# Kernel tuning notes

Measured on AMD Instinct MI355X. Metric: run time of the kernel, lower is better.

## Reference

```python
import jax, jax.numpy as jnp
import numpy as np

B, S, D, H = 2, 2048, 1024, 16
HD = D // H  # 64
MASK_VAL = -10000.0


def setup_inputs() -> dict:
    key = jax.random.key(0)
    ks = jax.random.split(key, 8)
    sc = 0.02
    q_features = jax.random.normal(ks[0], (B, S, D), jnp.float32)
    kv_features = jax.random.normal(ks[1], (B, S, D), jnp.float32)
    # causal mask, broadcastable (1,1,S,S)
    mask = jnp.tril(jnp.ones((S, S), jnp.bool_))[None, None]
    Wq = jax.random.normal(ks[2], (D, D), jnp.float32) * sc
    bq = jnp.zeros((D,), jnp.float32)
    Wkv = jax.random.normal(ks[3], (D, 2 * D), jnp.float32) * sc
    bkv = jnp.zeros((2 * D,), jnp.float32)
    Wp = jax.random.normal(ks[4], (D, D), jnp.float32) * sc
    bp = jnp.zeros((D,), jnp.float32)
    return {"q_features": q_features, "kv_features": kv_features, "mask": mask,
            "Wq": Wq, "bq": bq, "Wkv": Wkv, "bkv": bkv, "Wp": Wp, "bp": bp}


def _split_heads(t):
    # (B,S,D) -> (B,H,S,HD)
    return t.reshape(B, S, H, HD).transpose(0, 2, 1, 3)


def reference(q_features, kv_features, mask, Wq, bq, Wkv, bkv, Wp, bp):
    query = q_features @ Wq + bq            # (B,S,D)
    kv = kv_features @ Wkv + bkv            # (B,S,2D)
    key, value = jnp.split(kv, 2, axis=-1)
    q = _split_heads(query)                 # (B,H,S,HD)
    k = _split_heads(key)
    v = _split_heads(value)
    scores = jnp.einsum('bhqd,bhkd->bhqk', q, k) / jnp.sqrt(jnp.float32(HD))
    scores = jnp.where(mask, scores, jnp.asarray(MASK_VAL, scores.dtype))
    attn = jax.nn.softmax(scores, axis=-1)  # (B,H,S,S)
    out = jnp.einsum('bhqk,bhkd->bhqd', attn, v)
    out = out.transpose(0, 2, 1, 3).reshape(B, S, D)  # merge heads
    return out @ Wp + bp
```

## Files before the change

### kernel.cpp

```cpp
#include <hip/hip_runtime.h>

typedef unsigned short u16;
typedef unsigned int u32;
typedef __attribute__((ext_vector_type(4))) unsigned short us4;
typedef __attribute__((ext_vector_type(8))) unsigned short us8;
typedef __attribute__((ext_vector_type(8))) __bf16 bf16x8;
typedef __attribute__((ext_vector_type(4))) float floatx4;

#define S_ 2048
#define D_ 1024

__device__ __forceinline__ u16 f2bf(float f) {
  unsigned u = __builtin_bit_cast(unsigned, f);
  unsigned r = (u + 0x7fffu + ((u >> 16) & 1u)) >> 16;
  return (u16)r;
}

typedef const __attribute__((address_space(1))) u32* gas_t;
typedef __attribute__((address_space(3))) u32* las_t;
__device__ __forceinline__ void gload16(const u16* g, u16* l) {
  __builtin_amdgcn_global_load_lds((gas_t)g, (las_t)l, 16, 0, 0);
}

__global__ __launch_bounds__(256) void prep(
    const float* __restrict__ qf, const float* __restrict__ kvf,
    const float* __restrict__ Wq, const float* __restrict__ Wkv,
    const float* __restrict__ Wp, u16* __restrict__ qa, u16* __restrict__ kva,
    u16* __restrict__ Wqt, u16* __restrict__ Wkvt, u16* __restrict__ Wpt) {
  int bid = blockIdx.x, tid = threadIdx.x;
  if (bid < 4096) {
    const float* src = (bid < 2048) ? qf : kvf;
    u16* dst = (bid < 2048) ? qa : kva;
    size_t i = ((size_t)(bid & 2047) * 256 + tid) * 8;
    floatx4 a = *(const floatx4*)(src + i);
    floatx4 b = *(const floatx4*)(src + i + 4);
    us8 r;
#pragma unroll
    for (int j = 0; j < 4; j++) { r[j] = f2bf(a[j]); r[4 + j] = f2bf(b[j]); }
    *(us8*)(dst + i) = r;
  } else {
    int t = bid - 4096;
    const float* src; u16* dst; int R, C;
    if (t < 1024)      { src = Wq;  dst = Wqt;  R = 1024; C = 1024; }
    else if (t < 3072) { t -= 1024; src = Wkv; dst = Wkvt; R = 1024; C = 2048; }
    else               { t -= 3072; src = Wp;  dst = Wpt;  R = 1024; C = 1024; }
    int bx = t % (C >> 5), by = t / (C >> 5);
    __shared__ u16 tile[32][33];
    int tx = tid & 31, ty = tid >> 5;
    int x = bx * 32 + tx;
    for (int i = ty; i < 32; i += 8)
      tile[i][tx] = f2bf(src[(size_t)(by * 32 + i) * C + x]);
    __syncthreads();
    int ox = by * 32 + tx;
    for (int i = ty; i < 32; i += 8)
      dst[(size_t)(bx * 32 + i) * R + ox] = tile[tx][i];
  }
}

__device__ __forceinline__ void gemm_core(
    const u16* __restrict__ A, const u16* __restrict__ Bt,
    const float* __restrict__ bias, void* __restrict__ C0,
    u16* __restrict__ C1, int N, int mode, int n0, int m0,
    u16* As, u16* Bs) {
  int tid  = threadIdx.x;
  int wave = tid >> 6, lane = tid & 63;
  int quad = lane >> 4, l16 = lane & 15;
  int wr = wave >> 1, wc = wave & 1;
  const u16* Ag = A  + (size_t)(m0 + wave * 8 + (lane >> 3)) * 1024 + (lane & 7) * 8;
  const u16* Bg = Bt + (size_t)(n0 + wave * 8 + (lane >> 3)) * 1024 + (lane & 7) * 8;
  u16* Aw = As + wave * 8 * 64;
  u16* Bw = Bs + wave * 8 * 64;
  floatx4 acc[4][4] = {};
  for (int k0 = 0; k0 < 1024; k0 += 64) {
    if (k0) __syncthreads();
#pragma unroll
    for (int p = 0; p < 4; p++) {
      gload16(Ag + (size_t)p * 32 * 1024 + k0, Aw + p * 32 * 64);
      gload16(Bg + (size_t)p * 32 * 1024 + k0, Bw + p * 32 * 64);
    }
    __syncthreads();
#pragma unroll
    for (int kk = 0; kk < 2; kk++) {
      bf16x8 af[4], bf[4];
#pragma unroll
      for (int mt = 0; mt < 4; mt++)
        af[mt] = __builtin_bit_cast(bf16x8,
            *(const us8*)&As[(wr * 64 + mt * 16 + l16) * 64 + (kk * 4 + quad) * 8]);
#pragma unroll
      for (int nt = 0; nt < 4; nt++)
        bf[nt] = __builtin_bit_cast(bf16x8,
            *(const us8*)&Bs[(wc * 64 + nt * 16 + l16) * 64 + (kk * 4 + quad) * 8]);
#pragma unroll
      for (int mt = 0; mt < 4; mt++)
#pragma unroll
        for (int nt = 0; nt < 4; nt++)
          acc[mt][nt] = __builtin_amdgcn_mfma_f32_16x16x32_bf16(
              af[mt], bf[nt], acc[mt][nt], 0, 0, 0);
    }
  }
#pragma unroll
  for (int mt = 0; mt < 4; mt++) {
#pragma unroll
    for (int nt = 0; nt < 4; nt++) {
      int col  = n0 + wc * 64 + nt * 16 + l16;
      int rowq = m0 + wr * 64 + mt * 16 + quad * 4;
      float bv = bias[col];
      if (mode == 0) {
        u16* o = (u16*)C0;
#pragma unroll
        for (int r = 0; r < 4; r++)
          o[(size_t)(rowq + r) * N + col] = f2bf(acc[mt][nt][r] + bv);
      } else if (mode == 1) {
        float* o = (float*)C0;
#pragma unroll
        for (int r = 0; r < 4; r++)
          o[(size_t)(rowq + r) * N + col] = acc[mt][nt][r] + bv;
      } else {
        if (col < 1024) {
          u16* o = (u16*)C0;
#pragma unroll
          for (int r = 0; r < 4; r++)
            o[(size_t)(rowq + r) * 1024 + col] = f2bf(acc[mt][nt][r] + bv);
        } else {
          int vcol = col - 1024;
          int b = rowq >> 11, s0 = rowq & 2047;
          us4 pv;
#pragma unroll
          for (int r = 0; r < 4; r++) pv[r] = f2bf(acc[mt][nt][r] + bv);
          *(us4*)&C1[((size_t)(b * 1024 + vcol)) * (size_t)S_ + s0] = pv;
        }
      }
    }
  }
}

__global__ __launch_bounds__(256) void gemm_qkv(
    const u16* __restrict__ qa, const u16* __restrict__ kva,
    const u16* __restrict__ Wqt, const u16* __restrict__ Wkvt,
    const float* __restrict__ bq, const float* __restrict__ bkv,
    u16* __restrict__ Qb, u16* __restrict__ Kb, u16* __restrict__ Vt) {
  __shared__ __align__(16) u16 As[128 * 64];
  __shared__ __align__(16) u16 Bs[128 * 64];
  int bid = blockIdx.x;
  if (bid < 256) {
    gemm_core(qa, Wqt, bq, Qb, nullptr, 1024, 0,
              (bid & 7) * 128, (bid >> 3) * 128, As, Bs);
  } else {
    int lb = bid - 256;
    gemm_core(kva, Wkvt, bkv, Kb, Vt, 2048, 2,
              (lb & 15) * 128, (lb >> 4) * 128, As, Bs);
  }
}

__global__ __launch_bounds__(256) void gemm_out(
    const u16* __restrict__ AO, const u16* __restrict__ Wpt,
    const float* __restrict__ bp, float* __restrict__ out) {
  __shared__ __align__(16) u16 As[128 * 64];
  __shared__ __align__(16) u16 Bs[128 * 64];
  gemm_core(AO, Wpt, bp, out, nullptr, 1024, 1,
            (blockIdx.x & 7) * 128, (blockIdx.x >> 3) * 128, As, Bs);
}

__global__ __launch_bounds__(256) void attn_fwd(
    const u16* __restrict__ Q, const u16* __restrict__ Kb,
    const u16* __restrict__ Vt, u16* __restrict__ O) {
  __shared__ __align__(16) u16 Ks[2][64 * 64];
  __shared__ __align__(16) u16 Vs[2][64 * 64];
  __shared__ __align__(16) u16 Ps[4][16 * 72];
  int tid  = threadIdx.x;
  int wave = tid >> 6, lane = tid & 63;
  int quad = lane >> 4, l16 = lane & 15;
  int bh = blockIdx.x, b = bh >> 4, h = bh & 15;
  const size_t row0 = (size_t)b * S_;
  const u16* Kg = Kb + row0 * D_ + h * 64;
  const u16* Vg = Vt + ((size_t)b * 1024 + h * 64) * S_;
  int sr8 = tid >> 3, sc8 = tid & 7;

  for (int seg = 0; seg < 2; seg++) {
    int qt = seg ? (31 - blockIdx.y) : blockIdx.y;
    int qrow = qt * 64 + wave * 16 + l16;
    const u16* qp = Q + (row0 + qrow) * D_ + h * 64 + quad * 8;
    bf16x8 aqv[2];
    aqv[0] = __builtin_bit_cast(bf16x8, *(const us8*)(qp));
    aqv[1] = __builtin_bit_cast(bf16x8, *(const us8*)(qp + 32));

    float m_[4] = {-1e9f, -1e9f, -1e9f, -1e9f};
    float l_[4] = {0.f, 0.f, 0.f, 0.f};
    floatx4 o_[4] = {};

    __syncthreads();
#pragma unroll
    for (int rr = 0; rr < 2; rr++) {
      int r8 = sr8 + rr * 32;
      us8 k8 = *(const us8*)(Kg + (size_t)r8 * D_ + sc8 * 8);
      *(us8*)&Ks[0][r8 * 64 + ((sc8 ^ (r8 & 7)) << 3)] = k8;
      us8 v8 = *(const us8*)(Vg + (size_t)r8 * S_ + sc8 * 8);
      *(us8*)&Vs[0][r8 * 64 + ((sc8 ^ (r8 & 7)) << 3)] = v8;
    }

    for (int kb = 0; kb <= qt; kb++) {
      __syncthreads();
      int cur = kb & 1;
      bool pre = kb < qt;
      us8 pk0, pk1, pv0, pv1;
      if (pre) {
        int koff = (kb + 1) * 64;
        pk0 = *(const us8*)(Kg + (size_t)(koff + sr8) * D_ + sc8 * 8);
        pk1 = *(const us8*)(Kg + (size_t)(koff + sr8 + 32) * D_ + sc8 * 8);
        pv0 = *(const us8*)(Vg + (size_t)sr8 * S_ + koff + sc8 * 8);
        pv1 = *(const us8*)(Vg + (size_t)(sr8 + 32) * S_ + koff + sc8 * 8);
      }

      floatx4 s[4] = {};
#pragma unroll
      for (int kk = 0; kk < 2; kk++)
#pragma unroll
        for (int nt = 0; nt < 4; nt++) {
          int key = nt * 16 + l16;
          us8 kf = *(const us8*)&Ks[cur][key * 64 + (((kk * 4 + quad) ^ (l16 & 7)) << 3)];
          s[nt] = __builtin_amdgcn_mfma_f32_16x16x32_bf16(
              aqv[kk], __builtin_bit_cast(bf16x8, kf), s[nt], 0, 0, 0);
        }

      bool diag = (kb == qt);
#pragma unroll
      for (int nt = 0; nt < 4; nt++)
#pragma unroll
        for (int r = 0; r < 4; r++) {
          float v = s[nt][r] * 0.125f;
          if (diag) {
            int qg = wave * 16 + quad * 4 + r;
            int kg = nt * 16 + l16;
            if (kg > qg) v = -10000.0f;
          }
          s[nt][r] = v;
        }

      float mnew[4], alpha[4];
#pragma unroll
      for (int r = 0; r < 4; r++) {
        float rm = fmaxf(fmaxf(s[0][r], s[1][r]), fmaxf(s[2][r], s[3][r]));
        rm = fmaxf(rm, __shfl_xor(rm, 1));
        rm = fmaxf(rm, __shfl_xor(rm, 2));
        rm = fmaxf(rm, __shfl_xor(rm, 4));
        rm = fmaxf(rm, __shfl_xor(rm, 8));
        mnew[r] = fmaxf(m_[r], rm);
        alpha[r] = __expf(m_[r] - mnew[r]);
        m_[r] = mnew[r];
      }

#pragma unroll
      for (int nt = 0; nt < 4; nt++)
#pragma unroll
        for (int r = 0; r < 4; r++) {
          float p = __expf(s[nt][r] - mnew[r]);
          s[nt][r] = p;
          Ps[wave][(quad * 4 + r) * 72 + nt * 16 + l16] = f2bf(p);
        }
#pragma unroll
      for (int r = 0; r < 4; r++) {
        float rs = s[0][r] + s[1][r] + s[2][r] + s[3][r];
        rs += __shfl_xor(rs, 1);
        rs += __shfl_xor(rs, 2);
        rs += __shfl_xor(rs, 4);
        rs += __shfl_xor(rs, 8);
        l_[r] = l_[r] * alpha[r] + rs;
        o_[0][r] *= alpha[r];
        o_[1][r] *= alpha[r];
        o_[2][r] *= alpha[r];
        o_[3][r] *= alpha[r];
      }

#pragma unroll
      for (int kk = 0; kk < 2; kk++) {
        us8 pa = *(const us8*)&Ps[wave][l16 * 72 + (kk * 4 + quad) * 8];
        bf16x8 pav = __builtin_bit_cast(bf16x8, pa);
#pragma unroll
        for (int nt = 0; nt < 4; nt++) {
          int hd = nt * 16 + l16;
          us8 vf = *(const us8*)&Vs[cur][hd * 64 + (((kk * 4 + quad) ^ (l16 & 7)) << 3)];
          o_[nt] = __builtin_amdgcn_mfma_f32_16x16x32_bf16(
              pav, __builtin_bit_cast(bf16x8, vf), o_[nt], 0, 0, 0);
        }
      }

      if (pre) {
        int nxt = cur ^ 1;
        *(us8*)&Ks[nxt][sr8 * 64 + ((sc8 ^ (sr8 & 7)) << 3)] = pk0;
        *(us8*)&Ks[nxt][(sr8 + 32) * 64 + ((sc8 ^ (sr8 & 7)) << 3)] = pk1;
        *(us8*)&Vs[nxt][sr8 * 64 + ((sc8 ^ (sr8 & 7)) << 3)] = pv0;
        *(us8*)&Vs[nxt][(sr8 + 32) * 64 + ((sc8 ^ (sr8 & 7)) << 3)] = pv1;
      }
    }

#pragma unroll
    for (int nt = 0; nt < 4; nt++) {
      int col = h * 64 + nt * 16 + l16;
#pragma unroll
      for (int r = 0; r < 4; r++) {
        size_t row = row0 + qt * 64 + wave * 16 + quad * 4 + r;
        O[row * D_ + col] = f2bf(o_[nt][r] / l_[r]);
      }
    }
  }
}

extern "C" void kernel_launch(void* const* d_in, const int* in_sizes, int n_in,
                              void* d_out, int out_size, void* d_ws, size_t ws_size,
                              hipStream_t stream) {
  const float* qf  = (const float*)d_in[0];
  const float* kvf = (const float*)d_in[1];
  const float* Wq  = (const float*)d_in[3];
  const float* bq  = (const float*)d_in[4];
  const float* Wkv = (const float*)d_in[5];
  const float* bkv = (const float*)d_in[6];
  const float* Wp  = (const float*)d_in[7];
  const float* bp  = (const float*)d_in[8];

  char* ws = (char*)d_ws;
  const size_t MB = 1048576;
  u16* kva  = (u16*)(ws);
  u16* AO   = (u16*)(ws);
  u16* Kbp  = (u16*)(ws + 8 * MB);
  u16* Vtp  = (u16*)(ws + 16 * MB);
  u16* Wqt  = (u16*)(ws + 24 * MB);
  u16* Wkvt = (u16*)(ws + 26 * MB);
  u16* Wpt  = (u16*)(ws + 30 * MB);
  u16* qa   = (u16*)d_out;
  u16* Qb   = (u16*)d_out + (size_t)4 * 1048576;

  prep<<<8192, 256, 0, stream>>>(qf, kvf, Wq, Wkv, Wp, qa, kva, Wqt, Wkvt, Wpt);
  gemm_qkv<<<768, 256, 0, stream>>>(qa, kva, Wqt, Wkvt, bq, bkv, Qb, Kbp, Vtp);
  attn_fwd<<<dim3(32, 16), 256, 0, stream>>>(Qb, Kbp, Vtp, AO);
  gemm_out<<<256, 256, 0, stream>>>(AO, Wpt, bp, (float*)d_out);
}
```

Baseline: 252.7 us.

## Fold softmax scale into Q projection, use exp2, retile attention and output GEMM

The Q projection epilogue now multiplies by log2(e)/sqrt(64), so attention drops the per-score multiply and uses the hardware exp2 instruction. Attention runs one query tile per block with a grid of 32x32 instead of two balanced segments per block, and it uses single-buffered K/V with an extra barrier. The output GEMM is templated to 64x128 tiles and launches 512 blocks for better CU occupancy. Other small changes are round-half-up bf16 conversion for P and a reciprocal instead of a divide. Dropping the causal load-balancing pairing may leave the workload across blocks uneven, and the tail rounds can idle CUs.

After: 267.1 us. +5.7%, slower.

```diff
diff --git a/kernel.cpp b/kernel.cpp
--- a/kernel.cpp
+++ b/kernel.cpp
@@ -9,11 +9,15 @@
 
 #define S_ 2048
 #define D_ 1024
+#define QSC 0.18033688f
 
 __device__ __forceinline__ u16 f2bf(float f) {
   unsigned u = __builtin_bit_cast(unsigned, f);
   unsigned r = (u + 0x7fffu + ((u >> 16) & 1u)) >> 16;
   return (u16)r;
+}
+__device__ __forceinline__ u16 f2bf_rhu(float f) {
+  return (u16)((__builtin_bit_cast(unsigned, f) + 0x8000u) >> 16);
 }
 
 typedef const __attribute__((address_space(1))) u32* gas_t;
@@ -57,11 +61,13 @@
   }
 }
 
+template <int TM, int TN, int MODE>
 __device__ __forceinline__ void gemm_core(
     const u16* __restrict__ A, const u16* __restrict__ Bt,
     const float* __restrict__ bias, void* __restrict__ C0,
-    u16* __restrict__ C1, int N, int mode, int n0, int m0,
-    u16* As, u16* Bs) {
+    u16* __restrict__ C1, int N, int n0, int m0,
+    u16* As, u16* Bs, float cscale) {
+  constexpr int MT = TM / 32, NT = TN / 32;
   int tid  = threadIdx.x;
   int wave = tid >> 6, lane = tid & 63;
   int quad = lane >> 4, l16 = lane & 15;
@@ -70,47 +76,48 @@
   const u16* Bg = Bt + (size_t)(n0 + wave * 8 + (lane >> 3)) * 1024 + (lane & 7) * 8;
   u16* Aw = As + wave * 8 * 64;
   u16* Bw = Bs + wave * 8 * 64;
-  floatx4 acc[4][4] = {};
+  floatx4 acc[MT][NT] = {};
   for (int k0 = 0; k0 < 1024; k0 += 64) {
     if (k0) __syncthreads();
 #pragma unroll
-    for (int p = 0; p < 4; p++) {
+    for (int p = 0; p < TM / 32; p++)
       gload16(Ag + (size_t)p * 32 * 1024 + k0, Aw + p * 32 * 64);
+#pragma unroll
+    for (int p = 0; p < TN / 32; p++)
       gload16(Bg + (size_t)p * 32 * 1024 + k0, Bw + p * 32 * 64);
-    }
     __syncthreads();
 #pragma unroll
     for (int kk = 0; kk < 2; kk++) {
-      bf16x8 af[4], bf[4];
-#pragma unroll
-      for (int mt = 0; mt < 4; mt++)
+      bf16x8 af[MT], bf[NT];
+#pragma unroll
+      for (int mt = 0; mt < MT; mt++)
         af[mt] = __builtin_bit_cast(bf16x8,
-            *(const us8*)&As[(wr * 64 + mt * 16 + l16) * 64 + (kk * 4 + quad) * 8]);
-#pragma unroll
-      for (int nt = 0; nt < 4; nt++)
+            *(const us8*)&As[(wr * (TM / 2) + mt * 16 + l16) * 64 + (kk * 4 + quad) * 8]);
+#pragma unroll
+      for (int nt = 0; nt < NT; nt++)
         bf[nt] = __builtin_bit_cast(bf16x8,
-            *(const us8*)&Bs[(wc * 64 + nt * 16 + l16) * 64 + (kk * 4 + quad) * 8]);
-#pragma unroll
-      for (int mt = 0; mt < 4; mt++)
-#pragma unroll
-        for (int nt = 0; nt < 4; nt++)
+            *(const us8*)&Bs[(wc * (TN / 2) + nt * 16 + l16) * 64 + (kk * 4 + quad) * 8]);
+#pragma unroll
+      for (int mt = 0; mt < MT; mt++)
+#pragma unroll
+        for (int nt = 0; nt < NT; nt++)
           acc[mt][nt] = __builtin_amdgcn_mfma_f32_16x16x32_bf16(
               af[mt], bf[nt], acc[mt][nt], 0, 0, 0);
     }
   }
 #pragma unroll
-  for (int mt = 0; mt < 4; mt++) {
-#pragma unroll
-    for (int nt = 0; nt < 4; nt++) {
-      int col  = n0 + wc * 64 + nt * 16 + l16;
-      int rowq = m0 + wr * 64 + mt * 16 + quad * 4;
+  for (int mt = 0; mt < MT; mt++) {
+#pragma unroll
+    for (int nt = 0; nt < NT; nt++) {
+      int col  = n0 + wc * (TN / 2) + nt * 16 + l16;
+      int rowq = m0 + wr * (TM / 2) + mt * 16 + quad * 4;
       float bv = bias[col];
-      if (mode == 0) {
+      if (MODE == 0) {
         u16* o = (u16*)C0;
 #pragma unroll
         for (int r = 0; r < 4; r++)
-          o[(size_t)(rowq + r) * N + col] = f2bf(acc[mt][nt][r] + bv);
-      } else if (mode == 1) {
+          o[(size_t)(rowq + r) * N + col] = f2bf((acc[mt][nt][r] + bv) * cscale);
+      } else if (MODE == 1) {
         float* o = (float*)C0;
 #pragma unroll
         for (int r = 0; r < 4; r++)
@@ -143,164 +150,160 @@
   __shared__ __align__(16) u16 Bs[128 * 64];
   int bid = blockIdx.x;
   if (bid < 256) {
-    gemm_core(qa, Wqt, bq, Qb, nullptr, 1024, 0,
-              (bid & 7) * 128, (bid >> 3) * 128, As, Bs);
+    gemm_core<128, 128, 0>(qa, Wqt, bq, Qb, nullptr, 1024,
+                           (bid & 7) * 128, (bid >> 3) * 128, As, Bs, QSC);
   } else {
     int lb = bid - 256;
-    gemm_core(kva, Wkvt, bkv, Kb, Vt, 2048, 2,
-              (lb & 15) * 128, (lb >> 4) * 128, As, Bs);
+    gemm_core<128, 128, 2>(kva, Wkvt, bkv, Kb, Vt, 2048,
+                           (lb & 15) * 128, (lb >> 4) * 128, As, Bs, 1.0f);
   }
 }
 
 __global__ __launch_bounds__(256) void gemm_out(
     const u16* __restrict__ AO, const u16* __restrict__ Wpt,
     const float* __restrict__ bp, float* __restrict__ out) {
-  __shared__ __align__(16) u16 As[128 * 64];
+  __shared__ __align__(16) u16 As[64 * 64];
   __shared__ __align__(16) u16 Bs[128 * 64];
-  gemm_core(AO, Wpt, bp, out, nullptr, 1024, 1,
-            (blockIdx.x & 7) * 128, (blockIdx.x >> 3) * 128, As, Bs);
+  gemm_core<64, 128, 1>(AO, Wpt, bp, out, nullptr, 1024,
+                        (blockIdx.x & 7) * 128, (blockIdx.x >> 3) * 64, As, Bs, 1.0f);
 }
 
 __global__ __launch_bounds__(256) void attn_fwd(
     const u16* __restrict__ Q, const u16* __restrict__ Kb,
     const u16* __restrict__ Vt, u16* __restrict__ O) {
-  __shared__ __align__(16) u16 Ks[2][64 * 64];
-  __shared__ __align__(16) u16 Vs[2][64 * 64];
+  __shared__ __align__(16) u16 Ks[64 * 64];
+  __shared__ __align__(16) u16 Vs[64 * 64];
   __shared__ __align__(16) u16 Ps[4][16 * 72];
   int tid  = threadIdx.x;
   int wave = tid >> 6, lane = tid & 63;
   int quad = lane >> 4, l16 = lane & 15;
   int bh = blockIdx.x, b = bh >> 4, h = bh & 15;
+  int qt = blockIdx.y;
   const size_t row0 = (size_t)b * S_;
   const u16* Kg = Kb + row0 * D_ + h * 64;
   const u16* Vg = Vt + ((size_t)b * 1024 + h * 64) * S_;
   int sr8 = tid >> 3, sc8 = tid & 7;
 
-  for (int seg = 0; seg < 2; seg++) {
-    int qt = seg ? (31 - blockIdx.y) : blockIdx.y;
-    int qrow = qt * 64 + wave * 16 + l16;
-    const u16* qp = Q + (row0 + qrow) * D_ + h * 64 + quad * 8;
-    bf16x8 aqv[2];
-    aqv[0] = __builtin_bit_cast(bf16x8, *(const us8*)(qp));
-    aqv[1] = __builtin_bit_cast(bf16x8, *(const us8*)(qp + 32));
-
-    float m_[4] = {-1e9f, -1e9f, -1e9f, -1e9f};
-    float l_[4] = {0.f, 0.f, 0.f, 0.f};
-    floatx4 o_[4] = {};
-
+  int qrow = qt * 64 + wave * 16 + l16;
+  const u16* qp = Q + (row0 + qrow) * D_ + h * 64 + quad * 8;
+  bf16x8 aqv[2];
+  aqv[0] = __builtin_bit_cast(bf16x8, *(const us8*)(qp));
+  aqv[1] = __builtin_bit_cast(bf16x8, *(const us8*)(qp + 32));
+
+  float m_[4] = {-1e9f, -1e9f, -1e9f, -1e9f};
+  float l_[4] = {0.f, 0.f, 0.f, 0.f};
+  floatx4 o_[4] = {};
+
+#pragma unroll
+  for (int rr = 0; rr < 2; rr++) {
+    int r8 = sr8 + rr * 32;
+    us8 k8 = *(const us8*)(Kg + (size_t)r8 * D_ + sc8 * 8);
+    *(us8*)&Ks[r8 * 64 + ((sc8 ^ (r8 & 7)) << 3)] = k8;
+    us8 v8 = *(const us8*)(Vg + (size_t)r8 * S_ + sc8 * 8);
+    *(us8*)&Vs[r8 * 64 + ((sc8 ^ (r8 & 7)) << 3)] = v8;
+  }
+
+  for (int kb = 0; kb <= qt; kb++) {
     __syncthreads();
-#pragma unroll
-    for (int rr = 0; rr < 2; rr++) {
-      int r8 = sr8 + rr * 32;
-      us8 k8 = *(const us8*)(Kg + (size_t)r8 * D_ + sc8 * 8);
-      *(us8*)&Ks[0][r8 * 64 + ((sc8 ^ (r8 & 7)) << 3)] = k8;
-      us8 v8 = *(const us8*)(Vg + (size_t)r8 * S_ + sc8 * 8);
-      *(us8*)&Vs[0][r8 * 64 + ((sc8 ^ (r8 & 7)) << 3)] = v8;
-    }
-
-    for (int kb = 0; kb <= qt; kb++) {
-      __syncthreads();
-      int cur = kb & 1;
-      bool pre = kb < qt;
-      us8 pk0, pk1, pv0, pv1;
-      if (pre) {
-        int koff = (kb + 1) * 64;
-        pk0 = *(const us8*)(Kg + (size_t)(koff + sr8) * D_ + sc8 * 8);
-        pk1 = *(const us8*)(Kg + (size_t)(koff + sr8 + 32) * D_ + sc8 * 8);
-        pv0 = *(const us8*)(Vg + (size_t)sr8 * S_ + koff + sc8 * 8);
-        pv1 = *(const us8*)(Vg + (size_t)(sr8 + 32) * S_ + koff + sc8 * 8);
+    bool pre = kb < qt;
+    us8 pk0, pk1, pv0, pv1;
+    if (pre) {
+      int koff = (kb + 1) * 64;
+      pk0 = *(const us8*)(Kg + (size_t)(koff + sr8) * D_ + sc8 * 8);
+      pk1 = *(const us8*)(Kg + (size_t)(koff + sr8 + 32) * D_ + sc8 * 8);
+      pv0 = *(const us8*)(Vg + (size_t)sr8 * S_ + koff + sc8 * 8);
+      pv1 = *(const us8*)(Vg + (size_t)(sr8 + 32) * S_ + koff + sc8 * 8);
+    }
+
+    floatx4 s[4] = {};
+#pragma unroll
+    for (int kk = 0; kk < 2; kk++)
+#pragma unroll
+      for (int nt = 0; nt < 4; nt++) {
+        int key = nt * 16 + l16;
+        us8 kf = *(const us8*)&Ks[key * 64 + (((kk * 4 + quad) ^ (l16 & 7)) << 3)];
+        s[nt] = __builtin_amdgcn_mfma_f32_16x16x32_bf16(
+            aqv[kk], __builtin_bit_cast(bf16x8, kf), s[nt], 0, 0, 0);
       }
 
-      floatx4 s[4] = {};
-#pragma unroll
-      for (int kk = 0; kk < 2; kk++)
-#pragma unroll
-        for (int nt = 0; nt < 4; nt++) {
-          int key = nt * 16 + l16;
-          us8 kf = *(const us8*)&Ks[cur][key * 64 + (((kk * 4 + quad) ^ (l16 & 7)) << 3)];
-          s[nt] = __builtin_amdgcn_mfma_f32_16x16x32_bf16(
-              aqv[kk], __builtin_bit_cast(bf16x8, kf), s[nt], 0, 0, 0);
+    if (kb == qt) {
+#pragma unroll
+      for (int nt = 0; nt < 4; nt++)
+#pragma unroll
+        for (int r = 0; r < 4; r++) {
+          int qg = wave * 16 + quad * 4 + r;
+          int kg = nt * 16 + l16;
+          if (kg > qg) s[nt][r] = -1e5f;
         }
-
-      bool diag = (kb == qt);
-#pragma unroll
-      for (int nt = 0; nt < 4; nt++)
-#pragma unroll
-        for (int r = 0; r < 4; r++) {
-          float v = s[nt][r] * 0.125f;
-          if (diag) {
-            int qg = wave * 16 + quad * 4 + r;
-            int kg = nt * 16 + l16;
-            if (kg > qg) v = -10000.0f;
-          }
-          s[nt][r] = v;
-        }
-
-      float mnew[4], alpha[4];
+    }
+
+    float mnew[4], alpha[4];
+#pragma unroll
+    for (int r = 0; r < 4; r++) {
+      float rm = fmaxf(fmaxf(s[0][r], s[1][r]), fmaxf(s[2][r], s[3][r]));
+      rm = fmaxf(rm, __shfl_xor(rm, 1));
+      rm = fmaxf(rm, __shfl_xor(rm, 2));
+      rm = fmaxf(rm, __shfl_xor(rm, 4));
+      rm = fmaxf(rm, __shfl_xor(rm, 8));
+      mnew[r] = fmaxf(m_[r], rm);
+      alpha[r] = __builtin_amdgcn_exp2f(m_[r] - mnew[r]);
+      m_[r] = mnew[r];
+    }
+
+#pragma unroll
+    for (int nt = 0; nt < 4; nt++)
 #pragma unroll
       for (int r = 0; r < 4; r++) {
-        float rm = fmaxf(fmaxf(s[0][r], s[1][r]), fmaxf(s[2][r], s[3][r]));
-        rm = fmaxf(rm, __shfl_xor(rm, 1));
-        rm = fmaxf(rm, __shfl_xor(rm, 2));
-        rm = fmaxf(rm, __shfl_xor(rm, 4));
-        rm = fmaxf(rm, __shfl_xor(rm, 8));
-        mnew[r] = fmaxf(m_[r], rm);
-        alpha[r] = __expf(m_[r] - mnew[r]);
-        m_[r] = mnew[r];
+        float p = __builtin_amdgcn_exp2f(s[nt][r] - mnew[r]);
+        s[nt][r] = p;
+        Ps[wave][(quad * 4 + r) * 72 + nt * 16 + l16] = f2bf_rhu(p);
       }
-
-#pragma unroll
-      for (int nt = 0; nt < 4; nt++)
-#pragma unroll
-        for (int r = 0; r < 4; r++) {
-          float p = __expf(s[nt][r] - mnew[r]);
-          s[nt][r] = p;
-          Ps[wave][(quad * 4 + r) * 72 + nt * 16 + l16] = f2bf(p);
-        }
-#pragma unroll
-      for (int r = 0; r < 4; r++) {
-        float rs = s[0][r] + s[1][r] + s[2][r] + s[3][r];
-        rs += __shfl_xor(rs, 1);
-        rs += __shfl_xor(rs, 2);
-        rs += __shfl_xor(rs, 4);
-        rs += __shfl_xor(rs, 8);
-        l_[r] = l_[r] * alpha[r] + rs;
-        o_[0][r] *= alpha[r];
-        o_[1][r] *= alpha[r];
-        o_[2][r] *= alpha[r];
-        o_[3][r] *= alpha[r];
+#pragma unroll
+    for (int r = 0; r < 4; r++) {
+      float rs = s[0][r] + s[1][r] + s[2][r] + s[3][r];
+      rs += __shfl_xor(rs, 1);
+      rs += __shfl_xor(rs, 2);
+      rs += __shfl_xor(rs, 4);
+      rs += __shfl_xor(rs, 8);
+      l_[r] = l_[r] * alpha[r] + rs;
+      o_[0][r] *= alpha[r];
+      o_[1][r] *= alpha[r];
+      o_[2][r] *= alpha[r];
+      o_[3][r] *= alpha[r];
+    }
+
+#pragma unroll
+    for (int kk = 0; kk < 2; kk++) {
+      us8 pa = *(const us8*)&Ps[wave][l16 * 72 + (kk * 4 + quad) * 8];
+      bf16x8 pav = __builtin_bit_cast(bf16x8, pa);
+#pragma unroll
+      for (int nt = 0; nt < 4; nt++) {
+        int hd = nt * 16 + l16;
+        us8 vf = *(const us8*)&Vs[hd * 64 + (((kk * 4 + quad) ^ (l16 & 7)) << 3)];
+        o_[nt] = __builtin_amdgcn_mfma_f32_16x16x32_bf16(
+            pav, __builtin_bit_cast(bf16x8, vf), o_[nt], 0, 0, 0);
       }
-
-#pragma unroll
-      for (int kk = 0; kk < 2; kk++) {
-        us8 pa = *(const us8*)&Ps[wave][l16 * 72 + (kk * 4 + quad) * 8];
-        bf16x8 pav = __builtin_bit_cast(bf16x8, pa);
-#pragma unroll
-        for (int nt = 0; nt < 4; nt++) {
-          int hd = nt * 16 + l16;
-          us8 vf = *(const us8*)&Vs[cur][hd * 64 + (((kk * 4 + quad) ^ (l16 & 7)) << 3)];
-          o_[nt] = __builtin_amdgcn_mfma_f32_16x16x32_bf16(
-              pav, __builtin_bit_cast(bf16x8, vf), o_[nt], 0, 0, 0);
-        }
-      }
-
-      if (pre) {
-        int nxt = cur ^ 1;
-        *(us8*)&Ks[nxt][sr8 * 64 + ((sc8 ^ (sr8 & 7)) << 3)] = pk0;
-        *(us8*)&Ks[nxt][(sr8 + 32) * 64 + ((sc8 ^ (sr8 & 7)) << 3)] = pk1;
-        *(us8*)&Vs[nxt][sr8 * 64 + ((sc8 ^ (sr8 & 7)) << 3)] = pv0;
-        *(us8*)&Vs[nxt][(sr8 + 32) * 64 + ((sc8 ^ (sr8 & 7)) << 3)] = pv1;
-      }
-    }
-
-#pragma unroll
-    for (int nt = 0; nt < 4; nt++) {
-      int col = h * 64 + nt * 16 + l16;
-#pragma unroll
-      for (int r = 0; r < 4; r++) {
-        size_t row = row0 + qt * 64 + wave * 16 + quad * 4 + r;
-        O[row * D_ + col] = f2bf(o_[nt][r] / l_[r]);
-      }
+    }
+
+    __syncthreads();
+    if (pre) {
+      *(us8*)&Ks[sr8 * 64 + ((sc8 ^ (sr8 & 7)) << 3)] = pk0;
+      *(us8*)&Ks[(sr8 + 32) * 64 + ((sc8 ^ (sr8 & 7)) << 3)] = pk1;
+      *(us8*)&Vs[sr8 * 64 + ((sc8 ^ (sr8 & 7)) << 3)] = pv0;
+      *(us8*)&Vs[(sr8 + 32) * 64 + ((sc8 ^ (sr8 & 7)) << 3)] = pv1;
+    }
+  }
+
+  float rl[4];
+#pragma unroll
+  for (int r = 0; r < 4; r++) rl[r] = __builtin_amdgcn_rcpf(l_[r]);
+#pragma unroll
+  for (int nt = 0; nt < 4; nt++) {
+    int col = h * 64 + nt * 16 + l16;
+#pragma unroll
+    for (int r = 0; r < 4; r++) {
+      size_t row = row0 + qt * 64 + wave * 16 + quad * 4 + r;
+      O[row * D_ + col] = f2bf(o_[nt][r] * rl[r]);
     }
   }
 }
@@ -331,6 +334,6 @@
 
   prep<<<8192, 256, 0, stream>>>(qf, kvf, Wq, Wkv, Wp, qa, kva, Wqt, Wkvt, Wpt);
   gemm_qkv<<<768, 256, 0, stream>>>(qa, kva, Wqt, Wkvt, bq, bkv, Qb, Kbp, Vtp);
-  attn_fwd<<<dim3(32, 16), 256, 0, stream>>>(Qb, Kbp, Vtp, AO);
-  gemm_out<<<256, 256, 0, stream>>>(AO, Wpt, bp, (float*)d_out);
-}
+  attn_fwd<<<dim3(32, 32), 256, 0, stream>>>(Qb, Kbp, Vtp, AO);
+  gemm_out<<<512, 256, 0, stream>>>(AO, Wpt, bp, (float*)d_out);
+}
```
